# Kernel tuning notes

Hardware: AMD Instinct MI355X
Metric: run time of the kernel (lower is better)

Reference implementation:

```python
import jax, jax.numpy as jnp
import numpy as np

C = 256
SCALE = 2
K = 3
GROUPS = 4


def _conv(x, w, b=None, groups=1, pad=0):
    y = jax.lax.conv_general_dilated(
        x, w, window_strides=(1, 1), padding=[(pad, pad), (pad, pad)],
        dimension_numbers=("NCHW", "OIHW", "NCHW"), feature_group_count=groups)
    if b is not None:
        y = y + b[None, :, None, None]
    return y


def _bn(x, g, b, m, v):
    # eval-mode BatchNorm2d, eps=1e-5
    scale = g / jnp.sqrt(v + 1e-5)
    return (x - m[None, :, None, None]) * scale[None, :, None, None] + b[None, :, None, None]


def _silu(x):
    return x * jax.nn.sigmoid(x)


def setup_inputs() -> dict:
    key = jax.random.key(0)
    ks = jax.random.split(key, 16)
    c = C
    s2k2 = SCALE ** 2 * K ** 2
    p = lambda k, shape, sc=0.05: jax.random.normal(k, shape, dtype=jnp.float32) * sc
    return {
        "x": jax.random.normal(ks[0], (8, c, 64, 64), dtype=jnp.float32),
        # kernel_compressor: 1x1, c -> c//2
        "Wkc": p(ks[1], (c // 2, c, 1, 1)), "bkc": p(ks[2], (c // 2,)),
        # kernel_predictor: 3x3 c//2 -> c//4, BN, SiLU, 1x1 -> s^2*k^2
        "Wkp1": p(ks[3], (c // 4, c // 2, 3, 3)), "bkp1": p(ks[4], (c // 4,)),
        "g1": 1.0 + p(ks[5], (c // 4,)), "be1": p(ks[6], (c // 4,)),
        "m1": p(ks[7], (c // 4,)), "v1": 1.0 + jax.random.uniform(ks[8], (c // 4,), dtype=jnp.float32),
        "Wkp2": p(ks[9], (s2k2, c // 4, 1, 1)), "bkp2": p(ks[10], (s2k2,)),
        # grouped 3x3 "deform" conv: c -> c, groups=4, no bias
        "Wdef": p(ks[11], (c, c // GROUPS, 3, 3)),
        # semantic gate
        "Wg1": p(ks[12], (c // 4, c, 1, 1)), "bg1": p(ks[13], (c // 4,)),
        "Wg2": p(ks[14], (c, c // 4, 1, 1)), "bg2": p(ks[15], (c,)),
    }


def reference(x, Wkc, bkc, Wkp1, bkp1, g1, be1, m1, v1, Wkp2, bkp2, Wdef, Wg1, bg1, Wg2, bg2):
    b, c, h, w = x.shape
    s, k = SCALE, K
    # --- dynamic reassembly kernel prediction ---
    comp = _conv(x, Wkc, bkc)                                    # (b, c/2, h, w)
    t = _silu(_bn(_conv(comp, Wkp1, bkp1, pad=1), g1, be1, m1, v1))
    kw = _conv(t, Wkp2, bkp2)                                    # (b, s^2*k^2, h, w)
    kw = kw.transpose(0, 2, 3, 1).reshape(b, h, w, s * s, k * k)
    kw = jax.nn.softmax(kw, axis=-1)
    # --- unfold (k x k patches, pad k//2), F.unfold ordering: kernel pos i*k+j ---
    xp = jnp.pad(x, ((0, 0), (0, 0), (1, 1), (1, 1)))
    patches = jnp.stack([xp[:, :, i:i + h, j:j + w]
                         for i in range(k) for j in range(k)], axis=-1)  # (b,c,h,w,k^2)
    kernel_out = jnp.einsum('bchwk,bhwsk->bhwsc', patches, kw)           # (b,h,w,s^2,c)
    kernel_out = kernel_out.transpose(0, 4, 1, 3, 2).reshape(b, c, h * s, w * s)
    # --- grouped conv branch + bilinear upsample (align_corners=False) ---
    enh = _conv(x, Wdef, None, groups=GROUPS, pad=1)
    up = jax.image.resize(enh, (b, c, h * s, w * s), method='linear')
    fused = kernel_out + up
    # --- SE-style semantic gate ---
    pooled = jnp.mean(fused, axis=(2, 3), keepdims=True)
    gate = jax.nn.sigmoid(_conv(_silu(_conv(pooled, Wg1, bg1)), Wg2, bg2))
    return fused * gate
```

## Files before the change

### kernel.cpp

```cpp
#include <hip/hip_runtime.h>
#include <hip/hip_bf16.h>

typedef __hip_bfloat16 bf16;
typedef __attribute__((ext_vector_type(8))) short short8;
typedef __attribute__((ext_vector_type(4))) float floatx4;

__device__ __forceinline__ float cvt(float v){ return v; }
__device__ __forceinline__ float cvt(bf16 v){ return __bfloat162float(v); }
__device__ __forceinline__ unsigned short f2bu(float f){
    union { float f; unsigned u; } uf; uf.f = f;
    unsigned u = uf.u;
    return (unsigned short)((u + 0x7FFFu + ((u>>16)&1u)) >> 16);
}
__device__ __forceinline__ float bu2f(unsigned short b){
    union { unsigned u; float f; } uf; uf.u = ((unsigned)b)<<16; return uf.f;
}
__device__ __forceinline__ floatx4 mfma16(short8 a, short8 b, floatx4 c){
    return __builtin_amdgcn_mfma_f32_16x16x32_bf16(a, b, c, 0, 0, 0);
}
__device__ __forceinline__ int swz8(int row, int part){
    return row*32 + ((part ^ ((row>>1)&3))<<3);
}

constexpr size_t O_KW    = 0;
constexpr size_t O_ENH   = O_KW    + 1179648;
constexpr size_t O_XBT   = O_ENH   + 8388608;
constexpr size_t O_COMPB = O_XBT   + 4194304;
constexpr size_t O_TB    = O_COMPB + 2097152;
constexpr size_t O_POOL  = O_TB    + 1048576;
constexpr size_t O_GATE  = O_POOL  + 2048;
constexpr size_t O_WKC   = O_GATE  + 2048;
constexpr size_t O_BKC   = O_WKC   + 32768;
constexpr size_t O_WKP1  = O_BKC   + 128;
constexpr size_t O_ALPHA = O_WKP1  + 73728;
constexpr size_t O_BETA  = O_ALPHA + 64;
constexpr size_t O_WKP2  = O_BETA  + 64;
constexpr size_t O_BKP2  = O_WKP2  + 2304;
constexpr size_t O_WDEF  = O_BKP2  + 64;
constexpr size_t O_WG1   = O_WDEF  + 147456;
constexpr size_t O_BG1   = O_WG1   + 16384;
constexpr size_t O_WG2   = O_BG1   + 64;
constexpr size_t O_BG2   = O_WG2   + 16384;
constexpr size_t O_FLAG  = O_BG2   + 256;
constexpr size_t O_WKCB  = (O_FLAG + 1 + 3) & ~(size_t)3;
constexpr size_t O_WKP1B = O_WKCB  + 16384;
constexpr size_t O_WDEFB = O_WKP1B + 36864;

__global__ __launch_bounds__(256) void kdet(const unsigned* __restrict__ w, float* flag)
{
    int hits = 0;
    for (int i = threadIdx.x; i < 16384; i += 256){
        unsigned v = w[i];
        hits += (((v >> 7) & 0xFFu) == 0xFFu) ? 1 : 0;
    }
    __shared__ int sh[256];
    sh[threadIdx.x] = hits;
    __syncthreads();
    for (int o = 128; o > 0; o >>= 1){
        if (threadIdx.x < o) sh[threadIdx.x] += sh[threadIdx.x + o];
        __syncthreads();
    }
    if (threadIdx.x == 0) flag[0] = (sh[0] > 0) ? 1.0f : 0.0f;
}

template<typename T>
__device__ __forceinline__ void k0_body(
    const T* Wkc, const T* bkc, const T* Wkp1, const T* bkp1,
    const T* g1, const T* be1, const T* m1, const T* v1,
    const T* Wkp2, const T* bkp2, const T* Wdef,
    const T* Wg1, const T* bg1, const T* Wg2, const T* bg2,
    float* ws)
{
    int i = blockIdx.x*256 + threadIdx.x;
    if (i < 32768){ ws[O_WKC+i] = cvt(Wkc[i]); return; }  i -= 32768;
    if (i < 128)  { ws[O_BKC+i] = cvt(bkc[i]); return; }  i -= 128;
    if (i < 73728){ ws[O_WKP1+i]= cvt(Wkp1[i]); return; } i -= 73728;
    if (i < 64){
        float a = cvt(g1[i]) / sqrtf(cvt(v1[i]) + 1e-5f);
        ws[O_ALPHA+i] = a;
        ws[O_BETA+i]  = (cvt(bkp1[i]) - cvt(m1[i]))*a + cvt(be1[i]);
        return;
    } i -= 64;
    if (i < 2304) { ws[O_WKP2+i] = cvt(Wkp2[i]); return; } i -= 2304;
    if (i < 36)   { ws[O_BKP2+i] = cvt(bkp2[i]); return; } i -= 36;
    if (i < 147456){ ws[O_WDEF+i]= cvt(Wdef[i]); return; } i -= 147456;
    if (i < 16384){ ws[O_WG1+i]  = cvt(Wg1[i]); return; }  i -= 16384;
    if (i < 64)   { ws[O_BG1+i]  = cvt(bg1[i]); return; }  i -= 64;
    if (i < 16384){ ws[O_WG2+i]  = cvt(Wg2[i]); return; }  i -= 16384;
    if (i < 256)  { ws[O_BG2+i]  = cvt(bg2[i]); return; }  i -= 256;
    if (i < 2048) { ws[O_POOL+i] = 0.f; return; }
}

__global__ __launch_bounds__(256) void k0_prep(
    const void* Wkc, const void* bkc, const void* Wkp1, const void* bkp1,
    const void* g1, const void* be1, const void* m1, const void* v1,
    const void* Wkp2, const void* bkp2, const void* Wdef,
    const void* Wg1, const void* bg1, const void* Wg2, const void* bg2,
    float* ws)
{
    if (ws[O_FLAG] > 0.5f)
        k0_body<float>((const float*)Wkc,(const float*)bkc,(const float*)Wkp1,(const float*)bkp1,
                       (const float*)g1,(const float*)be1,(const float*)m1,(const float*)v1,
                       (const float*)Wkp2,(const float*)bkp2,(const float*)Wdef,
                       (const float*)Wg1,(const float*)bg1,(const float*)Wg2,(const float*)bg2, ws);
    else
        k0_body<bf16>((const bf16*)Wkc,(const bf16*)bkc,(const bf16*)Wkp1,(const bf16*)bkp1,
                      (const bf16*)g1,(const bf16*)be1,(const bf16*)m1,(const bf16*)v1,
                      (const bf16*)Wkp2,(const bf16*)bkp2,(const bf16*)Wdef,
                      (const bf16*)Wg1,(const bf16*)bg1,(const bf16*)Wg2,(const bf16*)bg2, ws);
}

__global__ __launch_bounds__(256) void k0b_pack(float* ws)
{
    unsigned short* wkcb  = (unsigned short*)(ws + O_WKCB);
    unsigned short* wkp1b = (unsigned short*)(ws + O_WKP1B);
    unsigned short* wdefb = (unsigned short*)(ws + O_WDEFB);
    int i = blockIdx.x*256 + threadIdx.x;
    if (i < 32768){
        int kc = i>>12, cout = (i>>5)&127, cil = i&31;
        wkcb[i] = f2bu(ws[O_WKC + (size_t)cout*256 + kc*32 + cil]);
        return;
    } i -= 32768;
    if (i < 73728){
        int ch = i/18432, r = i - ch*18432;
        int kp = r>>11, cout = (r>>5)&63, cil = r&31;
        wkp1b[i] = f2bu(ws[O_WKP1 + ((size_t)cout*128 + ch*32 + cil)*9 + kp]);
        return;
    } i -= 73728;
    if (i < 147456){
        int g = i/36864, r1 = i - g*36864;
        int ch = r1/18432, r2 = r1 - ch*18432;
        int kp = r2>>11, cout = (r2>>5)&63, cil = r2&31;
        wdefb[i] = f2bu(ws[O_WDEF + (((size_t)(g*64+cout))*64 + ch*32 + cil)*9 + kp]);
    }
}

template<typename T>
__device__ __forceinline__ void xcvt_body(const T* __restrict__ x, unsigned short* __restrict__ xbt,
                                          float* lT)
{
    const int b = blockIdx.y;
    const int ci0 = (blockIdx.x & 3) * 64;
    const int pos0 = (blockIdx.x >> 2) * 64;
    const int lane = threadIdx.x & 63;
    const int wrow = threadIdx.x >> 6;
    for (int i = wrow; i < 64; i += 4)
        lT[i*65 + lane] = cvt(x[((size_t)(b*256 + ci0 + i))*4096 + pos0 + lane]);
    __syncthreads();
    for (int u = threadIdx.x; u < 2048; u += 256){
        const int pr = u >> 5, pc = u & 31;
        unsigned lo = f2bu(lT[(2*pc)*65 + pr]);
        unsigned hi = f2bu(lT[(2*pc+1)*65 + pr]);
        *(unsigned*)&xbt[((size_t)(b*4096) + pos0 + pr)*256 + ci0 + 2*pc] = lo | (hi<<16);
    }
}

__global__ __launch_bounds__(256) void xcvt(const void* x, unsigned short* xbt, const float* flag)
{
    __shared__ float lT[64*65];
    if (*flag > 0.5f) xcvt_body<float>((const float*)x, xbt, lT);
    else              xcvt_body<bf16>((const bf16*)x, xbt, lT);
}

__global__ __launch_bounds__(256) void k1_mfma(
    const unsigned short* __restrict__ xbt, const unsigned short* __restrict__ wb,
    const float* __restrict__ bias, unsigned short* __restrict__ compb)
{
    __shared__ __align__(16) short lA[128*32];
    __shared__ __align__(16) short lB[128*32];
    const int b = blockIdx.y, pos0 = blockIdx.x*128;
    const int tid = threadIdx.x;
    const int wave = tid>>6, lane = tid&63, q = lane>>4, r16 = lane&15;
    const int mh = (wave&1)*64, nh = (wave>>1)*64;
    floatx4 zero = {0.f,0.f,0.f,0.f};
    floatx4 acc[4][4];
    #pragma unroll
    for (int m=0;m<4;m++){ acc[m][0]=zero; acc[m][1]=zero; acc[m][2]=zero; acc[m][3]=zero; }

    for (int kc=0;kc<8;kc++){
        __syncthreads();
        {
            const short8* s = (const short8*)(wb + kc*4096);
            const int u0 = tid, u1 = tid + 256;
            *(short8*)&lA[swz8(u0>>2, u0&3)] = s[u0];
            *(short8*)&lA[swz8(u1>>2, u1&3)] = s[u1];
        }
        {
            #pragma unroll
            for (int k=0;k<2;k++){
                const int u = tid + k*256;
                const int p = u>>2, part = u&3;
                *(short8*)&lB[swz8(p, part)] =
                    *(const short8*)(xbt + ((size_t)(b*4096)+pos0+p)*256 + kc*32 + part*8);
            }
        }
        __syncthreads();
        short8 af[4], bfr[4];
        #pragma unroll
        for (int mt=0;mt<4;mt++) af[mt]  = *(const short8*)&lA[swz8(mh + mt*16 + r16, q)];
        #pragma unroll
        for (int nt=0;nt<4;nt++) bfr[nt] = *(const short8*)&lB[swz8(nh + nt*16 + r16, q)];
        #pragma unroll
        for (int mt=0;mt<4;mt++)
            #pragma unroll
            for (int nt=0;nt<4;nt++)
                acc[mt][nt] = mfma16(af[mt], bfr[nt], acc[mt][nt]);
    }
    #pragma unroll
    for (int mt=0;mt<4;mt++){
        const int cb = mh + mt*16 + q*4;
        const float b0=bias[cb], b1=bias[cb+1], b2=bias[cb+2], b3=bias[cb+3];
        #pragma unroll
        for (int nt=0;nt<4;nt++){
            const int pos = pos0 + nh + nt*16 + r16;
            floatx4 v = acc[mt][nt];
            uint2 pk;
            pk.x = (unsigned)f2bu(v.x+b0) | ((unsigned)f2bu(v.y+b1)<<16);
            pk.y = (unsigned)f2bu(v.z+b2) | ((unsigned)f2bu(v.w+b3)<<16);
            *(uint2*)(compb + ((size_t)(b*4096)+pos)*128 + cb) = pk;
        }
    }
}

__global__ __launch_bounds__(256) void conv3x3_all(
    const unsigned short* __restrict__ xbt, const unsigned short* __restrict__ compb,
    const unsigned short* __restrict__ wkp1b, const unsigned short* __restrict__ wdefb,
    const float* __restrict__ alpha, const float* __restrict__ beta,
    unsigned short* __restrict__ tb, float* __restrict__ enh)
{
    __shared__ __align__(16) short lX[6*66*32];
    __shared__ __align__(16) short lW[9*64*32];
    const int row0 = blockIdx.x*4, b = blockIdx.y, z = blockIdx.z;
    const bool isKP = (z == 0);
    const int g = isKP ? 0 : (z-1);
    const int CICH  = isKP ? 4 : 2;
    const int CITOT = isKP ? 128 : 256;
    const int cibase = g*64;
    const unsigned short* src  = isKP ? compb : xbt;
    const unsigned short* wsrc = isKP ? wkp1b : (wdefb + (size_t)g*36864);
    const int tid = threadIdx.x;
    const int wave = tid>>6, lane = tid&63, q = lane>>4, r16 = lane&15;
    floatx4 zero = {0.f,0.f,0.f,0.f};
    floatx4 acc[4][4];
    #pragma unroll
    for (int m=0;m<4;m++){ acc[m][0]=zero; acc[m][1]=zero; acc[m][2]=zero; acc[m][3]=zero; }

    {
        short8 zz = {0,0,0,0,0,0,0,0};
        short8* d = (short8*)lX;
        for (int i = tid; i < 1584; i += 256) d[i] = zz;
    }

    for (int ch = 0; ch < CICH; ch++){
        __syncthreads();
        {
            const short8* s = (const short8*)(wsrc + ch*18432);
            #pragma unroll
            for (int i=0;i<9;i++){
                const int u = tid + i*256;
                *(short8*)&lW[swz8(u>>2, u&3)] = s[u];
            }
        }
        {
            const int gc = tid>>2, part = tid&3;
            #pragma unroll
            for (int r=0;r<6;r++){
                const int gr = row0 - 1 + r;
                if ((unsigned)gr < 64u){
                    const unsigned short* sp = src +
                        ((size_t)(b*4096) + gr*64 + gc)*CITOT + cibase + ch*32 + part*8;
                    *(short8*)&lX[swz8(r*66 + 1 + gc, part)] = *(const short8*)sp;
                }
            }
        }
        __syncthreads();
        #pragma unroll
        for (int kp=0; kp<9; kp++){
            const int dr = kp/3, dc = kp - dr*3;
            short8 af[4], bfr[4];
            #pragma unroll
            for (int mt=0;mt<4;mt++)
                af[mt] = *(const short8*)&lW[swz8(kp*64 + mt*16 + r16, q)];
            #pragma unroll
            for (int nt=0;nt<4;nt++)
                bfr[nt] = *(const short8*)&lX[swz8((wave+dr)*66 + nt*16 + r16 + dc, q)];
            #pragma unroll
            for (int mt=0;mt<4;mt++)
                #pragma unroll
                for (int nt=0;nt<4;nt++)
                    acc[mt][nt] = mfma16(af[mt], bfr[nt], acc[mt][nt]);
        }
    }
    const int orow = row0 + wave;
    if (isKP){
        #pragma unroll
        for (int mt=0;mt<4;mt++){
            const int cb = mt*16 + q*4;
            const float a0=alpha[cb],a1=alpha[cb+1],a2=alpha[cb+2],a3=alpha[cb+3];
            const float e0=beta[cb],e1=beta[cb+1],e2=beta[cb+2],e3=beta[cb+3];
            #pragma unroll
            for (int nt=0;nt<4;nt++){
                const int pos = orow*64 + nt*16 + r16;
                floatx4 v = acc[mt][nt];
                float z0=v.x*a0+e0, z1=v.y*a1+e1, z2=v.z*a2+e2, z3=v.w*a3+e3;
                z0 = z0/(1.f+expf(-z0)); z1 = z1/(1.f+expf(-z1));
                z2 = z2/(1.f+expf(-z2)); z3 = z3/(1.f+expf(-z3));
                uint2 pk;
                pk.x = (unsigned)f2bu(z0) | ((unsigned)f2bu(z1)<<16);
                pk.y = (unsigned)f2bu(z2) | ((unsigned)f2bu(z3)<<16);
                *(uint2*)(tb + ((size_t)(b*4096)+pos)*64 + cb) = pk;
            }
        }
    } else {
        #pragma unroll
        for (int mt=0;mt<4;mt++){
            #pragma unroll
            for (int nt=0;nt<4;nt++){
                const int pos = orow*64 + nt*16 + r16;
                floatx4 v = acc[mt][nt];
                float* op = enh + ((size_t)(b*256) + g*64 + mt*16 + q*4)*4096 + pos;
                op[0]=v.x; op[4096]=v.y; op[8192]=v.z; op[12288]=v.w;
            }
        }
    }
}

__global__ __launch_bounds__(128) void k3_kpred(
    const unsigned short* __restrict__ tb, const float* __restrict__ W,
    const float* __restrict__ bias, float* __restrict__ kw)
{
    __shared__ float wl[2304];
    __shared__ float bl[36];
    for (int i=threadIdx.x;i<2304;i+=128) wl[i]=W[i];
    if (threadIdx.x<36) bl[threadIdx.x]=bias[threadIdx.x];
    __syncthreads();
    const int gid = blockIdx.x*128 + threadIdx.x;
    const unsigned short* tp = tb + (size_t)gid*64;
    float acc[36];
    #pragma unroll
    for (int o=0;o<36;o++) acc[o]=bl[o];
    #pragma unroll
    for (int c8=0;c8<8;c8++){
        uint4 pk = *(const uint4*)(tp + c8*8);
        unsigned u[4] = {pk.x, pk.y, pk.z, pk.w};
        float f[8];
        #pragma unroll
        for (int j=0;j<4;j++){
            f[2*j]   = bu2f((unsigned short)(u[j]&0xFFFFu));
            f[2*j+1] = bu2f((unsigned short)(u[j]>>16));
        }
        #pragma unroll
        for (int jj=0;jj<8;jj++){
            const int ci = c8*8+jj;
            #pragma unroll
            for (int o=0;o<36;o++) acc[o] += f[jj]*wl[o*64+ci];
        }
    }
    float* op = kw + (size_t)gid*36;
    #pragma unroll
    for (int s=0;s<4;s++){
        float mx = acc[s*9];
        #pragma unroll
        for (int k=1;k<9;k++) mx = fmaxf(mx, acc[s*9+k]);
        float e[9]; float sum=0.f;
        #pragma unroll
        for (int k=0;k<9;k++){ e[k]=expf(acc[s*9+k]-mx); sum+=e[k]; }
        float inv = 1.f/sum;
        #pragma unroll
        for (int k=0;k<9;k++) op[s*9+k] = e[k]*inv;
    }
}

template<typename T>
__device__ __forceinline__ void k5_body(
    const T* __restrict__ x, const float* __restrict__ kw,
    const float* __restrict__ enh, float* __restrict__ out,
    float* __restrict__ pooled, float* kwl)
{
    const int hi = blockIdx.x & 63;
    const int b  = blockIdx.x >> 6;
    const int c0 = blockIdx.y * 32;
    for (int i=threadIdx.x;i<2304;i+=256){
        int wi = i/36, r = i - wi*36;
        kwl[wi*37+r] = kw[((size_t)(b*4096 + hi*64 + wi))*36 + r];
    }
    __syncthreads();
    const int wi = threadIdx.x & 63;
    const int cl = threadIdx.x >> 6;
    float kreg[36];
    #pragma unroll
    for (int r=0;r<36;r++) kreg[r] = kwl[wi*37+r];

    const bool vx0 = wi>0, vx2 = wi<63;
    const bool vy0 = hi>0, vy2 = hi<63;
    const int rm = vy0? hi-1 : 0;
    const int rp = vy2? hi+1 : 63;
    const int par = wi&1;
    const int mA = wi>>1, mB = 32+mA;
    float wc0, wc1; int a0,a1,b0c,b1c;
    if (par==0){ wc0=0.25f; wc1=0.75f; a0=(mA>0)?mA-1:0; a1=mA;   b0c=mB-1; b1c=mB; }
    else       { wc0=0.75f; wc1=0.25f; a0=mA;            a1=mA+1; b0c=mB;   b1c=(mB<63)?mB+1:63; }
    const int y0 = hi*2;

    for (int c = c0+cl; c < c0+32; c += 4){
        const T* xc = x + ((size_t)(b*256)+c)*4096;
        float v[9];
        v[0] = (vy0&&vx0)? cvt(xc[(hi-1)*64+wi-1]) : 0.f;
        v[1] = (vy0)     ? cvt(xc[(hi-1)*64+wi  ]) : 0.f;
        v[2] = (vy0&&vx2)? cvt(xc[(hi-1)*64+wi+1]) : 0.f;
        v[3] = (vx0)     ? cvt(xc[ hi   *64+wi-1]) : 0.f;
        v[4] =             cvt(xc[ hi   *64+wi  ]);
        v[5] = (vx2)     ? cvt(xc[ hi   *64+wi+1]) : 0.f;
        v[6] = (vy2&&vx0)? cvt(xc[(hi+1)*64+wi-1]) : 0.f;
        v[7] = (vy2)     ? cvt(xc[(hi+1)*64+wi  ]) : 0.f;
        v[8] = (vy2&&vx2)? cvt(xc[(hi+1)*64+wi+1]) : 0.f;
        float ko[4];
        #pragma unroll
        for (int s=0;s<4;s++){
            float a = 0.f;
            #pragma unroll
            for (int k=0;k<9;k++) a += v[k]*kreg[s*9+k];
            ko[s]=a;
        }
        const float* ec = enh + ((size_t)(b*256)+c)*4096;
        const float* er0 = ec + rm*64;
        const float* er1 = ec + hi*64;
        const float* er2 = ec + rp*64;
        float uA0 = wc0*er0[a0]+wc1*er0[a1];
        float uB0 = wc0*er0[b0c]+wc1*er0[b1c];
        float uA1 = wc0*er1[a0]+wc1*er1[a1];
        float uB1 = wc0*er1[b0c]+wc1*er1[b1c];
        float uA2 = wc0*er2[a0]+wc1*er2[a1];
        float uB2 = wc0*er2[b0c]+wc1*er2[b1c];
        float up00 = 0.25f*uA0 + 0.75f*uA1;
        float up01 = 0.25f*uB0 + 0.75f*uB1;
        float up10 = 0.75f*uA1 + 0.25f*uA2;
        float up11 = 0.75f*uB1 + 0.25f*uB2;
        float o00 = ko[0]+up00, o01 = ko[1]+up01, o10 = ko[2]+up10, o11 = ko[3]+up11;
        float* o = out + (((size_t)(b*256)+c)*128 + y0)*128;
        o[wi]      = o00;
        o[64+wi]   = o01;
        o[128+wi]  = o10;
        o[192+wi]  = o11;
        float ps = (o00+o01) + (o10+o11);
        #pragma unroll
        for (int off=32;off>0;off>>=1) ps += __shfl_down(ps, off, 64);
        if (wi==0) atomicAdd(&pooled[b*256 + c], ps);
    }
}

__global__ __launch_bounds__(256) void k5_fuse(
    const void* x, const float* kw, const float* enh, float* out,
    float* pooled, const float* flag)
{
    __shared__ float kwl[64*37];
    if (*flag > 0.5f) k5_body<float>((const float*)x, kw, enh, out, pooled, kwl);
    else              k5_body<bf16>((const bf16*)x, kw, enh, out, pooled, kwl);
}

__global__ __launch_bounds__(256) void k7_gate(
    const float* __restrict__ pooled,
    const float* __restrict__ Wg1, const float* __restrict__ bg1,
    const float* __restrict__ Wg2, const float* __restrict__ bg2,
    float* __restrict__ gate)
{
    const int b = blockIdx.x;
    __shared__ float pl[256];
    __shared__ float hid[64];
    pl[threadIdx.x] = pooled[b*256+threadIdx.x] * (1.f/16384.f);
    __syncthreads();
    if (threadIdx.x < 64){
        float a = bg1[threadIdx.x];
        const float* w = Wg1 + (size_t)threadIdx.x*256;
        for (int c=0;c<256;c++) a += w[c]*pl[c];
        hid[threadIdx.x] = a/(1.f+expf(-a));
    }
    __syncthreads();
    float a = bg2[threadIdx.x];
    const float* w = Wg2 + (size_t)threadIdx.x*64;
    for (int j=0;j<64;j++) a += w[j]*hid[j];
    gate[b*256+threadIdx.x] = 1.f/(1.f+expf(-a));
}

__global__ __launch_bounds__(256) void k8_scale(
    float* __restrict__ out, const float* __restrict__ gate)
{
    const size_t gid = (size_t)blockIdx.x*256 + threadIdx.x;
    const float g = gate[gid>>12];
    float4* p = (float4*)out;
    float4 v = p[gid];
    v.x*=g; v.y*=g; v.z*=g; v.w*=g;
    p[gid] = v;
}

extern "C" void kernel_launch(void* const* d_in, const int* in_sizes, int n_in,
                              void* d_out, int out_size, void* d_ws, size_t ws_size,
                              hipStream_t stream)
{
    float* ws = (float*)d_ws;
    float* out = (float*)d_out;
    unsigned short* xbt   = (unsigned short*)(ws + O_XBT);
    unsigned short* compb = (unsigned short*)(ws + O_COMPB);
    unsigned short* tb    = (unsigned short*)(ws + O_TB);
    unsigned short* wkcb  = (unsigned short*)(ws + O_WKCB);
    unsigned short* wkp1b = (unsigned short*)(ws + O_WKP1B);
    unsigned short* wdefb = (unsigned short*)(ws + O_WDEFB);

    kdet<<<1, 256, 0, stream>>>((const unsigned*)d_in[1], ws + O_FLAG);
    k0_prep<<<1140, 256, 0, stream>>>(d_in[1],d_in[2],d_in[3],d_in[4],d_in[5],d_in[6],d_in[7],d_in[8],
                                      d_in[9],d_in[10],d_in[11],d_in[12],d_in[13],d_in[14],d_in[15], ws);
    k0b_pack<<<992, 256, 0, stream>>>(ws);
    xcvt<<<dim3(256,8), 256, 0, stream>>>(d_in[0], xbt, ws+O_FLAG);
    k1_mfma<<<dim3(32,8), 256, 0, stream>>>(xbt, wkcb, ws+O_BKC, compb);
    conv3x3_all<<<dim3(16,8,5), 256, 0, stream>>>(xbt, compb, wkp1b, wdefb,
                                                  ws+O_ALPHA, ws+O_BETA, tb, ws+O_ENH);
    k3_kpred<<<256, 128, 0, stream>>>(tb, ws+O_WKP2, ws+O_BKP2, ws+O_KW);
    k5_fuse<<<dim3(512,8), 256, 0, stream>>>(d_in[0], ws+O_KW, ws+O_ENH, out, ws+O_POOL, ws+O_FLAG);
    k7_gate<<<8, 256, 0, stream>>>(ws+O_POOL, ws+O_WG1, ws+O_BG1, ws+O_WG2, ws+O_BG2, ws+O_GATE);
    k8_scale<<<32768, 256, 0, stream>>>(out, ws+O_GATE);
}
```

Measured before the change: 381.2 us.

## Process two pixels per thread in fuse kernel with vector loads and stores

Reworks the fused reassembly/upsample kernel so each lane handles two adjacent input columns. It loads 3x4 neighbourhoods and pairs of enh values with wide loads, writes float2 outputs, and reduces the pooled sum over 32 lanes. The block covers 64 channels instead of 32, halving the grid and the redundant kw loads into shared memory. This doubles the kernel-weight registers per thread (72 floats), which may cut occupancy, and adds edge-case select logic.

Result: faster. 352.2 us (-7.6%).

```diff
diff --git a/kernel.cpp b/kernel.cpp
--- a/kernel.cpp
+++ b/kernel.cpp
@@ -20,6 +20,15 @@
 }
 __device__ __forceinline__ int swz8(int row, int part){
     return row*32 + ((part ^ ((row>>1)&3))<<3);
+}
+template<typename T>
+__device__ __forceinline__ void ld4(const T* p, float& o0, float& o1, float& o2, float& o3){
+    T t[4]; __builtin_memcpy(t, p, 4*sizeof(T));
+    o0=cvt(t[0]); o1=cvt(t[1]); o2=cvt(t[2]); o3=cvt(t[3]);
+}
+__device__ __forceinline__ void ld2f(const float* p, float& o0, float& o1){
+    float t[2]; __builtin_memcpy(t, p, 8);
+    o0=t[0]; o1=t[1];
 }
 
 constexpr size_t O_KW    = 0;
@@ -379,73 +388,97 @@
 {
     const int hi = blockIdx.x & 63;
     const int b  = blockIdx.x >> 6;
-    const int c0 = blockIdx.y * 32;
+    const int c0 = blockIdx.y * 64;
     for (int i=threadIdx.x;i<2304;i+=256){
         int wi = i/36, r = i - wi*36;
         kwl[wi*37+r] = kw[((size_t)(b*4096 + hi*64 + wi))*36 + r];
     }
     __syncthreads();
-    const int wi = threadIdx.x & 63;
-    const int cl = threadIdx.x >> 6;
-    float kreg[36];
-    #pragma unroll
-    for (int r=0;r<36;r++) kreg[r] = kwl[wi*37+r];
-
-    const bool vx0 = wi>0, vx2 = wi<63;
+    const int lane = threadIdx.x & 63;
+    const int wv   = threadIdx.x >> 6;
+    const int a    = lane & 31;
+    const int hsel = lane >> 5;
+
+    float k0r[36], k1r[36];
+    #pragma unroll
+    for (int r=0;r<36;r++) k0r[r] = kwl[(2*a)*37+r];
+    #pragma unroll
+    for (int r=0;r<36;r++) k1r[r] = kwl[(2*a+1)*37+r];
+
     const bool vy0 = hi>0, vy2 = hi<63;
     const int rm = vy0? hi-1 : 0;
     const int rp = vy2? hi+1 : 63;
-    const int par = wi&1;
-    const int mA = wi>>1, mB = 32+mA;
-    float wc0, wc1; int a0,a1,b0c,b1c;
-    if (par==0){ wc0=0.25f; wc1=0.75f; a0=(mA>0)?mA-1:0; a1=mA;   b0c=mB-1; b1c=mB; }
-    else       { wc0=0.75f; wc1=0.25f; a0=mA;            a1=mA+1; b0c=mB;   b1c=(mB<63)?mB+1:63; }
     const int y0 = hi*2;
-
-    for (int c = c0+cl; c < c0+32; c += 4){
-        const T* xc = x + ((size_t)(b*256)+c)*4096;
-        float v[9];
-        v[0] = (vy0&&vx0)? cvt(xc[(hi-1)*64+wi-1]) : 0.f;
-        v[1] = (vy0)     ? cvt(xc[(hi-1)*64+wi  ]) : 0.f;
-        v[2] = (vy0&&vx2)? cvt(xc[(hi-1)*64+wi+1]) : 0.f;
-        v[3] = (vx0)     ? cvt(xc[ hi   *64+wi-1]) : 0.f;
-        v[4] =             cvt(xc[ hi   *64+wi  ]);
-        v[5] = (vx2)     ? cvt(xc[ hi   *64+wi+1]) : 0.f;
-        v[6] = (vy2&&vx0)? cvt(xc[(hi+1)*64+wi-1]) : 0.f;
-        v[7] = (vy2)     ? cvt(xc[(hi+1)*64+wi  ]) : 0.f;
-        v[8] = (vy2&&vx2)? cvt(xc[(hi+1)*64+wi+1]) : 0.f;
-        float ko[4];
+    const bool e0 = (a==0), e31 = (a==31);
+    const int xb = e0 ? 0 : (e31 ? 60 : (2*a-1));
+    const int eAb = e0 ? 0 : a-1;
+    const int eBb = 31 + a;
+    const int eAr = a+1;
+    const int eBr = e31 ? 63 : 33+a;
+
+    for (int it=0; it<8; ++it){
+        const int c = c0 + (wv<<1) + hsel + (it<<3);
+        const T* xc = x + ((size_t)(b*256)+c)*4096 + hi*64 + xb;
+        float g[3][4];
+        ld4(xc, g[1][0], g[1][1], g[1][2], g[1][3]);
+        if (vy0) ld4(xc-64, g[0][0], g[0][1], g[0][2], g[0][3]);
+        else     { g[0][0]=0.f; g[0][1]=0.f; g[0][2]=0.f; g[0][3]=0.f; }
+        if (vy2) ld4(xc+64, g[2][0], g[2][1], g[2][2], g[2][3]);
+        else     { g[2][0]=0.f; g[2][1]=0.f; g[2][2]=0.f; g[2][3]=0.f; }
+        float w0[3][4];
+        #pragma unroll
+        for (int i=0;i<3;i++){
+            float g0=g[i][0], g1=g[i][1], g2=g[i][2], g3=g[i][3];
+            w0[i][0] = e0 ? 0.f : (e31 ? g1 : g0);
+            w0[i][1] = e0 ? g0  : (e31 ? g2 : g1);
+            w0[i][2] = e0 ? g1  : (e31 ? g3 : g2);
+            w0[i][3] = e0 ? g2  : (e31 ? 0.f : g3);
+        }
+        float ko[2][4];
         #pragma unroll
         for (int s=0;s<4;s++){
-            float a = 0.f;
-            #pragma unroll
-            for (int k=0;k<9;k++) a += v[k]*kreg[s*9+k];
-            ko[s]=a;
+            float a0c = 0.f, a1c = 0.f;
+            #pragma unroll
+            for (int i=0;i<3;i++){
+                a0c += w0[i][0]*k0r[s*9+3*i] + w0[i][1]*k0r[s*9+3*i+1] + w0[i][2]*k0r[s*9+3*i+2];
+                a1c += w0[i][1]*k1r[s*9+3*i] + w0[i][2]*k1r[s*9+3*i+1] + w0[i][3]*k1r[s*9+3*i+2];
+            }
+            ko[0][s]=a0c; ko[1][s]=a1c;
         }
         const float* ec = enh + ((size_t)(b*256)+c)*4096;
-        const float* er0 = ec + rm*64;
-        const float* er1 = ec + hi*64;
-        const float* er2 = ec + rp*64;
-        float uA0 = wc0*er0[a0]+wc1*er0[a1];
-        float uB0 = wc0*er0[b0c]+wc1*er0[b1c];
-        float uA1 = wc0*er1[a0]+wc1*er1[a1];
-        float uB1 = wc0*er1[b0c]+wc1*er1[b1c];
-        float uA2 = wc0*er2[a0]+wc1*er2[a1];
-        float uB2 = wc0*er2[b0c]+wc1*er2[b1c];
-        float up00 = 0.25f*uA0 + 0.75f*uA1;
-        float up01 = 0.25f*uB0 + 0.75f*uB1;
-        float up10 = 0.75f*uA1 + 0.25f*uA2;
-        float up11 = 0.75f*uB1 + 0.25f*uB2;
-        float o00 = ko[0]+up00, o01 = ko[1]+up01, o10 = ko[2]+up10, o11 = ko[3]+up11;
+        float hAe[3], hAo[3], hBe[3], hBo[3];
+        const int rows[3] = {rm, hi, rp};
+        #pragma unroll
+        for (int i=0;i<3;i++){
+            const float* er = ec + rows[i]*64;
+            float fA0, fA1; ld2f(er + eAb, fA0, fA1);
+            float vAl = fA0, vAc = e0 ? fA0 : fA1;
+            float vAr = er[eAr];
+            float fB0, fB1; ld2f(er + eBb, fB0, fB1);
+            float vBr = er[eBr];
+            hAe[i] = 0.25f*vAl + 0.75f*vAc;
+            hAo[i] = 0.75f*vAc + 0.25f*vAr;
+            hBe[i] = 0.25f*fB0 + 0.75f*fB1;
+            hBo[i] = 0.75f*fB1 + 0.25f*vBr;
+        }
+        float uAe0 = 0.25f*hAe[0] + 0.75f*hAe[1], uAe1 = 0.75f*hAe[1] + 0.25f*hAe[2];
+        float uAo0 = 0.25f*hAo[0] + 0.75f*hAo[1], uAo1 = 0.75f*hAo[1] + 0.25f*hAo[2];
+        float uBe0 = 0.25f*hBe[0] + 0.75f*hBe[1], uBe1 = 0.75f*hBe[1] + 0.25f*hBe[2];
+        float uBo0 = 0.25f*hBo[0] + 0.75f*hBo[1], uBo1 = 0.75f*hBo[1] + 0.25f*hBo[2];
+        float o00 = ko[0][0]+uAe0, o01 = ko[1][0]+uAo0;
+        float o02 = ko[0][1]+uBe0, o03 = ko[1][1]+uBo0;
+        float o10 = ko[0][2]+uAe1, o11 = ko[1][2]+uAo1;
+        float o12 = ko[0][3]+uBe1, o13 = ko[1][3]+uBo1;
         float* o = out + (((size_t)(b*256)+c)*128 + y0)*128;
-        o[wi]      = o00;
-        o[64+wi]   = o01;
-        o[128+wi]  = o10;
-        o[192+wi]  = o11;
-        float ps = (o00+o01) + (o10+o11);
-        #pragma unroll
-        for (int off=32;off>0;off>>=1) ps += __shfl_down(ps, off, 64);
-        if (wi==0) atomicAdd(&pooled[b*256 + c], ps);
+        *(float2*)(o + 2*a)        = make_float2(o00, o01);
+        *(float2*)(o + 64 + 2*a)   = make_float2(o02, o03);
+        *(float2*)(o + 128 + 2*a)  = make_float2(o10, o11);
+        *(float2*)(o + 192 + 2*a)  = make_float2(o12, o13);
+        float ps = (o00+o01) + (o02+o03) + (o10+o11) + (o12+o13);
+        ps += __shfl_down(ps,16,32); ps += __shfl_down(ps, 8,32);
+        ps += __shfl_down(ps, 4,32); ps += __shfl_down(ps, 2,32);
+        ps += __shfl_down(ps, 1,32);
+        if (a==0) atomicAdd(&pooled[b*256 + c], ps);
     }
 }
 
@@ -515,7 +548,7 @@
     conv3x3_all<<<dim3(16,8,5), 256, 0, stream>>>(xbt, compb, wkp1b, wdefb,
                                                   ws+O_ALPHA, ws+O_BETA, tb, ws+O_ENH);
     k3_kpred<<<256, 128, 0, stream>>>(tb, ws+O_WKP2, ws+O_BKP2, ws+O_KW);
-    k5_fuse<<<dim3(512,8), 256, 0, stream>>>(d_in[0], ws+O_KW, ws+O_ENH, out, ws+O_POOL, ws+O_FLAG);
+    k5_fuse<<<dim3(512,4), 256, 0, stream>>>(d_in[0], ws+O_KW, ws+O_ENH, out, ws+O_POOL, ws+O_FLAG);
     k7_gate<<<8, 256, 0, stream>>>(ws+O_POOL, ws+O_WG1, ws+O_BG1, ws+O_WG2, ws+O_BG2, ws+O_GATE);
     k8_scale<<<32768, 256, 0, stream>>>(out, ws+O_GATE);
 }
```
